# Performance work log

Hardware: AMD Instinct MI355X
Metric: run time of the kernel (lower is better)

## Reference

```python
import jax, jax.numpy as jnp
import numpy as np

B, N, F, C, K = 4, 8192, 128, 64, 16


def setup_inputs() -> dict:
    key = jax.random.key(0)
    ks = jax.random.split(key, 24)
    s = 0.05
    rn = lambda k, shape: (jax.random.normal(k, shape, jnp.float32) * s)
    return {
        "features": jax.random.normal(ks[0], (B, N, F), jnp.float32),
        "positions": jax.random.normal(ks[1], (B, N, 3), jnp.float32),
        "batch": jnp.repeat(jnp.arange(B, dtype=jnp.int32), N),
        "num_neighbors": K,
        # linear encoder (F -> C)
        "W_enc": rn(ks[2], (F, C)), "b_enc": jnp.zeros((C,), jnp.float32),
        # point-transformer q/k/v projections (C -> C)
        "Wq": rn(ks[3], (C, C)), "bq": jnp.zeros((C,), jnp.float32),
        "Wk": rn(ks[4], (C, C)), "bk": jnp.zeros((C,), jnp.float32),
        "Wv": rn(ks[5], (C, C)), "bv": jnp.zeros((C,), jnp.float32),
        # positional encoding MLP: 3 -> C -> C (ReLU)
        "Wp1": rn(ks[6], (3, C)), "bp1": jnp.zeros((C,), jnp.float32),
        "Wp2": rn(ks[7], (C, C)), "bp2": jnp.zeros((C,), jnp.float32),
        # attention MLP gamma: C -> C -> C (ReLU)
        "Wa1": rn(ks[8], (C, C)), "ba1": jnp.zeros((C,), jnp.float32),
        "Wa2": rn(ks[9], (C, C)), "ba2": jnp.zeros((C,), jnp.float32),
        # linear decoder (C -> F)
        "W_dec": rn(ks[10], (C, F)), "b_dec": jnp.zeros((F,), jnp.float32),
    }


def reference(features, positions, batch, num_neighbors,
              W_enc, b_enc, Wq, bq, Wk, bk, Wv, bv,
              Wp1, bp1, Wp2, bp2, Wa1, ba1, Wa2, ba2, W_dec, b_dec):
    # linear encode: [B,N,F] -> [B,N,C]
    x = features @ W_enc + b_enc
    q = x @ Wq + bq
    k = x @ Wk + bk
    v = x @ Wv + bv

    def per_cloud(pos, qi, ki, vi):
        # kNN via pairwise squared distances (self included, dist 0)
        sq = jnp.sum(pos * pos, axis=-1)                      # [N]
        d2 = sq[:, None] + sq[None, :] - 2.0 * (pos @ pos.T)  # [N,N]
        idx = jax.lax.top_k(-d2, num_neighbors)[1]            # [N,K]
        kj = ki[idx]                                          # [N,K,C] gather
        vj = vi[idx]                                          # [N,K,C]
        rel = pos[:, None, :] - pos[idx]                      # [N,K,3]
        # positional encoding delta = MLP(p_i - p_j)
        delta = jax.nn.relu(rel @ Wp1 + bp1) @ Wp2 + bp2      # [N,K,C]
        # vector attention: gamma(q_i - k_j + delta), softmax over K neighbors
        a = qi[:, None, :] - kj + delta
        a = jax.nn.relu(a @ Wa1 + ba1) @ Wa2 + ba2
        w = jax.nn.softmax(a, axis=1)                         # [N,K,C]
        return jnp.sum(w * (vj + delta), axis=1)              # [N,C]

    y = jax.vmap(per_cloud)(positions, q, k, v)               # [B,N,C]
    out = y @ W_dec + b_dec + features                        # decode + residual
    return (out, positions, batch)
```

## Files before the change

### kernel.cpp

```cpp
#include <hip/hip_runtime.h>
#include <hip/hip_bf16.h>

#define NPTS 32768
#define NPC  8192
#define KNN  16
#define CH   64
#define FDIM 128
#define EMPTYKEY 0x7F7FFFFFu

typedef __bf16 bf16;
typedef __bf16 bf16x2 __attribute__((ext_vector_type(2)));
typedef __bf16 bf16x8 __attribute__((ext_vector_type(8)));
typedef float  f32x4  __attribute__((ext_vector_type(4)));

__global__ __launch_bounds__(256) void k_encode(
    const float* __restrict__ feat,
    const float* __restrict__ Wenc, const float* __restrict__ benc,
    const float* __restrict__ Wq, const float* __restrict__ bq,
    const float* __restrict__ Wk, const float* __restrict__ bk,
    const float* __restrict__ Wv, const float* __restrict__ bv,
    float* __restrict__ qo, float* __restrict__ ko, float* __restrict__ vo)
{
    __shared__ float xs[4][CH];
    int t = threadIdx.x;
    int c = t & 63, pl = t >> 6;
    size_t pt = (size_t)blockIdx.x * 4 + pl;
    const float* fr = feat + pt * FDIM;
    float acc = benc[c];
#pragma unroll 8
    for (int f4 = 0; f4 < 32; ++f4) {
        float4 fv = *reinterpret_cast<const float4*>(fr + f4 * 4);
        acc += fv.x * Wenc[(f4*4+0)*CH + c];
        acc += fv.y * Wenc[(f4*4+1)*CH + c];
        acc += fv.z * Wenc[(f4*4+2)*CH + c];
        acc += fv.w * Wenc[(f4*4+3)*CH + c];
    }
    xs[pl][c] = acc;
    __syncthreads();
    float aq = bq[c], ak = bk[c], av = bv[c];
#pragma unroll 4
    for (int m = 0; m < CH; ++m) {
        float xm = xs[pl][m];
        aq += xm * Wq[m*CH + c];
        ak += xm * Wk[m*CH + c];
        av += xm * Wv[m*CH + c];
    }
    qo[pt*CH + c] = aq; ko[pt*CH + c] = ak; vo[pt*CH + c] = av;
}

__global__ __launch_bounds__(256, 4) void k_knn(
    const float* __restrict__ pos, unsigned* __restrict__ wsK)
{
    __shared__ float4 sp[1024];
    __shared__ unsigned sbuf[256 * 17];

    int t = threadIdx.x;
    int blk = blockIdx.x;
    int slice = blk & 7;
    int qg = (blk >> 3) & 31;
    int cloud = blk >> 8;
    const float* pc = pos + (size_t)cloud * NPC * 3;
    int jbase = slice << 10;

    {
        const float4* src = reinterpret_cast<const float4*>(pc + (size_t)jbase * 3);
        float4 a = src[t*3+0], b1 = src[t*3+1], c1 = src[t*3+2];
        sp[t*4+0] = make_float4(a.x,  a.y,  a.z,  0.f);
        sp[t*4+1] = make_float4(a.w,  b1.x, b1.y, 0.f);
        sp[t*4+2] = make_float4(b1.z, b1.w, c1.x, 0.f);
        sp[t*4+3] = make_float4(c1.y, c1.z, c1.w, 0.f);
    }
    __syncthreads();

    int qi = (qg << 8) + t;
    float myx = pc[qi*3+0], myy = pc[qi*3+1], myz = pc[qi*3+2];

    unsigned arr[16];
#pragma unroll
    for (int r = 0; r < 16; ++r) arr[r] = EMPTYKEY;
    float thrf = __uint_as_float(EMPTYKEY & 0xFFFFE000u);
    int cnt = 0;
    int base = t * 17;

    for (int g = 0; g < 1024; g += 4) {
        float d2v[4];
#pragma unroll
        for (int u = 0; u < 4; ++u) {
            float4 p = sp[g + u];
            float dx = myx - p.x, dy = myy - p.y, dz = myz - p.z;
            d2v[u] = dx*dx + dy*dy + dz*dz;
        }
        float m4 = fminf(fminf(d2v[0], d2v[1]), fminf(d2v[2], d2v[3]));
        if (__any(m4 <= thrf)) {
#pragma unroll
            for (int u = 0; u < 4; ++u) {
                if (d2v[u] <= thrf) {
                    sbuf[base + cnt] = (__float_as_uint(d2v[u]) & 0xFFFFE000u)
                                       | (unsigned)(jbase + g + u);
                    ++cnt;
                }
            }
            if (__any(cnt >= 13)) {
#pragma unroll
                for (int b = 0; b < 16; ++b) {
                    unsigned key = (b < cnt) ? sbuf[base + b] : EMPTYKEY;
#pragma unroll
                    for (int r = 0; r < 16; ++r) {
                        unsigned lo = min(key, arr[r]);
                        unsigned hi = max(key, arr[r]);
                        arr[r] = lo; key = hi;
                    }
                }
                cnt = 0;
                thrf = __uint_as_float(arr[15] & 0xFFFFE000u);
            }
        }
    }
#pragma unroll
    for (int b = 0; b < 16; ++b) {
        unsigned key = (b < cnt) ? sbuf[base + b] : EMPTYKEY;
#pragma unroll
        for (int r = 0; r < 16; ++r) {
            unsigned lo = min(key, arr[r]);
            unsigned hi = max(key, arr[r]);
            arr[r] = lo; key = hi;
        }
    }
    size_t gq = (size_t)cloud * NPC + qi;
#pragma unroll
    for (int r = 0; r < 16; ++r) wsK[(size_t)(slice*16 + r)*NPTS + gq] = arr[r];
}

__global__ __launch_bounds__(64) void k_merge(
    const unsigned* __restrict__ wsK, int* __restrict__ idxout,
    const float* __restrict__ Wp2, const float* __restrict__ Wa1,
    const float* __restrict__ Wa2, bf16* __restrict__ wpk)
{
    __shared__ unsigned kk[64][137];
    int t = threadIdx.x;
    size_t q = (size_t)blockIdx.x * 64 + t;
#pragma unroll
    for (int l = 0; l < 8; ++l) {
#pragma unroll
        for (int r = 0; r < 16; ++r)
            kk[t][l*17 + r] = wsK[(size_t)(l*16 + r)*NPTS + q];
        kk[t][l*17 + 16] = 0xFFFFFFFFu;
    }

    unsigned h0=0,h1=0,h2=0,h3=0,h4=0,h5=0,h6=0,h7=0;
    int* o = idxout + q * KNN;
    for (int r = 0; r < KNN; ++r) {
        unsigned best = 0xFFFFFFFFu; int bl = 0; unsigned k;
        k = kk[t][0*17 + h0]; if (k < best) { best = k; bl = 0; }
        k = kk[t][1*17 + h1]; if (k < best) { best = k; bl = 1; }
        k = kk[t][2*17 + h2]; if (k < best) { best = k; bl = 2; }
        k = kk[t][3*17 + h3]; if (k < best) { best = k; bl = 3; }
        k = kk[t][4*17 + h4]; if (k < best) { best = k; bl = 4; }
        k = kk[t][5*17 + h5]; if (k < best) { best = k; bl = 5; }
        k = kk[t][6*17 + h6]; if (k < best) { best = k; bl = 6; }
        k = kk[t][7*17 + h7]; if (k < best) { best = k; bl = 7; }
        o[r] = (int)(best & 0x1FFFu);
        h0 += (bl == 0); h1 += (bl == 1); h2 += (bl == 2); h3 += (bl == 3);
        h4 += (bl == 4); h5 += (bl == 5); h6 += (bl == 6); h7 += (bl == 7);
    }

    if (blockIdx.x == 0) {
        int lane = t;
        int mlane = lane & 15, kgrp = lane >> 4;
        const float* Ws[3] = {Wp2, Wa1, Wa2};
        bf16x8* ow = reinterpret_cast<bf16x8*>(wpk);
        for (int gmm = 0; gmm < 3; ++gmm) {
#pragma unroll
            for (int nt = 0; nt < 4; ++nt) {
#pragma unroll
                for (int kt = 0; kt < 2; ++kt) {
                    bf16x8 v;
#pragma unroll
                    for (int j = 0; j < 8; ++j)
                        v[j] = (bf16)Ws[gmm][(kt*32 + kgrp*8 + j)*CH + nt*16 + mlane];
                    ow[(gmm*8 + nt*2 + kt)*64 + lane] = v;
                }
            }
        }
    }
}

__device__ __forceinline__ void wave_gemm(
    const bf16* At, f32x4 acc[4][4], const bf16x8* __restrict__ wpk,
    int w, int lane)
{
    int kgrp = lane >> 4;
    bf16x8 wf[4][2];
#pragma unroll
    for (int nt = 0; nt < 4; ++nt)
#pragma unroll
        for (int kt = 0; kt < 2; ++kt)
            wf[nt][kt] = wpk[(nt*2 + kt)*64 + lane];
#pragma unroll
    for (int mt = 0; mt < 4; ++mt) {
        int row = w*64 + mt*16 + (lane & 15);
        const bf16* rb = At + row*CH;
        int sw = row & 7;
        bf16x8 a0 = *reinterpret_cast<const bf16x8*>(rb + ((kgrp     ^ sw) * 8));
        bf16x8 a1 = *reinterpret_cast<const bf16x8*>(rb + (((4+kgrp) ^ sw) * 8));
#pragma unroll
        for (int nt = 0; nt < 4; ++nt) {
            acc[mt][nt] = __builtin_amdgcn_mfma_f32_16x16x32_bf16(a0, wf[nt][0], acc[mt][nt], 0, 0, 0);
            acc[mt][nt] = __builtin_amdgcn_mfma_f32_16x16x32_bf16(a1, wf[nt][1], acc[mt][nt], 0, 0, 0);
        }
    }
}

__global__ __launch_bounds__(128, 3) void k_attn(
    const float* __restrict__ pos, const int* __restrict__ nidx,
    const float* __restrict__ qg, const float* __restrict__ kg, const float* __restrict__ vg,
    const float* __restrict__ Wp1, const float* __restrict__ bp1,
    const float* __restrict__ bp2, const float* __restrict__ ba1,
    const float* __restrict__ ba2, const bf16* __restrict__ wpkg,
    float* __restrict__ yout)
{
    __shared__ bf16 At[128 * CH];

    int t = threadIdx.x;
    int w = t >> 6, lane = t & 63;
    int mlane = lane & 15, kgrp = lane >> 4;
    size_t p0 = (size_t)blockIdx.x * 8;
    size_t cbase = (p0 >> 13) << 13;
    const bf16x8* wpk = reinterpret_cast<const bf16x8*>(wpkg);

    {
        int p = t >> 4, j = t & 15;
        size_t gp = p0 + p;
        int nbr = nidx[gp*KNN + j];
        size_t gn = cbase + (size_t)nbr;
        float rx = pos[gp*3+0] - pos[gn*3+0];
        float ry = pos[gp*3+1] - pos[gn*3+1];
        float rz = pos[gp*3+2] - pos[gn*3+2];
        float h[CH];
#pragma unroll
        for (int c4 = 0; c4 < 16; ++c4) {
            float4 w0 = *reinterpret_cast<const float4*>(Wp1 + 0*CH + c4*4);
            float4 w1 = *reinterpret_cast<const float4*>(Wp1 + 1*CH + c4*4);
            float4 w2 = *reinterpret_cast<const float4*>(Wp1 + 2*CH + c4*4);
            float4 bb = *reinterpret_cast<const float4*>(bp1 + c4*4);
            h[c4*4+0] = fmaxf(rx*w0.x + ry*w1.x + rz*w2.x + bb.x, 0.f);
            h[c4*4+1] = fmaxf(rx*w0.y + ry*w1.y + rz*w2.y + bb.y, 0.f);
            h[c4*4+2] = fmaxf(rx*w0.z + ry*w1.z + rz*w2.z + bb.z, 0.f);
            h[c4*4+3] = fmaxf(rx*w0.w + ry*w1.w + rz*w2.w + bb.w, 0.f);
        }
#pragma unroll
        for (int ch = 0; ch < 8; ++ch) {
            bf16x8 v;
#pragma unroll
            for (int e = 0; e < 8; ++e) v[e] = (bf16)h[ch*8 + e];
            *reinterpret_cast<bf16x8*>(&At[t*CH + (ch ^ (t & 7)) * 8]) = v;
        }
    }

    f32x4 acc[4][4];

#pragma unroll
    for (int nt = 0; nt < 4; ++nt) {
        float b = bp2[nt*16 + mlane];
#pragma unroll
        for (int mt = 0; mt < 4; ++mt) { acc[mt][nt][0]=b; acc[mt][nt][1]=b; acc[mt][nt][2]=b; acc[mt][nt][3]=b; }
    }
    wave_gemm(At, acc, wpk, w, lane);

    bf16x2 vdp[4][4][2];
#pragma unroll
    for (int mt = 0; mt < 4; ++mt) {
        size_t gp = p0 + (size_t)(w*4 + mt);
        int nb[4];
#pragma unroll
        for (int reg = 0; reg < 4; ++reg)
            nb[reg] = nidx[gp*KNN + kgrp*4 + reg];
#pragma unroll
        for (int nt = 0; nt < 4; ++nt) {
            int c = nt*16 + mlane;
            float qv = qg[gp*CH + c];
            float vdf[4];
#pragma unroll
            for (int reg = 0; reg < 4; ++reg) {
                float dlt = acc[mt][nt][reg];
                size_t gr = cbase + (size_t)nb[reg];
                float kv = kg[gr*CH + c];
                float vv = vg[gr*CH + c];
                int row = w*64 + mt*16 + kgrp*4 + reg;
                int off = row*CH + (((c >> 3) ^ (row & 7)) * 8) + (c & 7);
                At[off] = (bf16)(qv - kv + dlt);
                vdf[reg] = vv + dlt;
            }
            bf16x2 lo2; lo2[0] = (bf16)vdf[0]; lo2[1] = (bf16)vdf[1];
            bf16x2 hi2; hi2[0] = (bf16)vdf[2]; hi2[1] = (bf16)vdf[3];
            vdp[mt][nt][0] = lo2;
            vdp[mt][nt][1] = hi2;
        }
    }

#pragma unroll
    for (int nt = 0; nt < 4; ++nt) {
        float b = ba1[nt*16 + mlane];
#pragma unroll
        for (int mt = 0; mt < 4; ++mt) { acc[mt][nt][0]=b; acc[mt][nt][1]=b; acc[mt][nt][2]=b; acc[mt][nt][3]=b; }
    }
    wave_gemm(At, acc, wpk + 512, w, lane);
#pragma unroll
    for (int mt = 0; mt < 4; ++mt) {
#pragma unroll
        for (int nt = 0; nt < 4; ++nt) {
            int c = nt*16 + mlane;
#pragma unroll
            for (int reg = 0; reg < 4; ++reg) {
                int row = w*64 + mt*16 + kgrp*4 + reg;
                int off = row*CH + (((c >> 3) ^ (row & 7)) * 8) + (c & 7);
                At[off] = (bf16)fmaxf(acc[mt][nt][reg], 0.f);
            }
        }
    }

#pragma unroll
    for (int nt = 0; nt < 4; ++nt) {
        float b = ba2[nt*16 + mlane];
#pragma unroll
        for (int mt = 0; mt < 4; ++mt) { acc[mt][nt][0]=b; acc[mt][nt][1]=b; acc[mt][nt][2]=b; acc[mt][nt][3]=b; }
    }
    wave_gemm(At, acc, wpk + 1024, w, lane);

#pragma unroll
    for (int mt = 0; mt < 4; ++mt) {
        size_t gp = p0 + (size_t)(w*4 + mt);
#pragma unroll
        for (int nt = 0; nt < 4; ++nt) {
            int c = nt*16 + mlane;
            float m = fmaxf(fmaxf(acc[mt][nt][0], acc[mt][nt][1]),
                            fmaxf(acc[mt][nt][2], acc[mt][nt][3]));
            m = fmaxf(m, __shfl_xor(m, 16));
            m = fmaxf(m, __shfl_xor(m, 32));
            float e[4], s = 0.f;
#pragma unroll
            for (int reg = 0; reg < 4; ++reg) { e[reg] = __expf(acc[mt][nt][reg] - m); s += e[reg]; }
            s += __shfl_xor(s, 16);
            s += __shfl_xor(s, 32);
            float num = 0.f;
            num += e[0] * (float)vdp[mt][nt][0][0];
            num += e[1] * (float)vdp[mt][nt][0][1];
            num += e[2] * (float)vdp[mt][nt][1][0];
            num += e[3] * (float)vdp[mt][nt][1][1];
            num += __shfl_xor(num, 16);
            num += __shfl_xor(num, 32);
            if (kgrp == 0) yout[gp*CH + c] = num / s;
        }
    }
}

__global__ __launch_bounds__(256) void k_decode(
    const float* __restrict__ y, const float* __restrict__ Wd, const float* __restrict__ bd,
    const float* __restrict__ feat, const float* __restrict__ pos,
    const int* __restrict__ batch, float* __restrict__ out)
{
    int t = threadIdx.x;
    int f = t & 127, pl = t >> 7;
    size_t pt = (size_t)blockIdx.x * 2 + pl;
    const float* yr = y + pt*CH;
    float acc = bd[f] + feat[pt*FDIM + f];
#pragma unroll
    for (int c4 = 0; c4 < 16; ++c4) {
        float4 yv = *reinterpret_cast<const float4*>(yr + c4*4);
        acc += yv.x * Wd[(c4*4+0)*FDIM + f];
        acc += yv.y * Wd[(c4*4+1)*FDIM + f];
        acc += yv.z * Wd[(c4*4+2)*FDIM + f];
        acc += yv.w * Wd[(c4*4+3)*FDIM + f];
    }
    out[pt*FDIM + f] = acc;

    int i = blockIdx.x * 256 + t;
    if (i < NPTS*3) out[(size_t)NPTS*FDIM + i] = pos[i];
    if (i < NPTS)   out[(size_t)NPTS*FDIM + NPTS*3 + i] = (float)batch[i];
}

extern "C" void kernel_launch(void* const* d_in, const int* in_sizes, int n_in,
                              void* d_out, int out_size, void* d_ws, size_t ws_size,
                              hipStream_t stream)
{
    const float* feat  = (const float*)d_in[0];
    const float* pos   = (const float*)d_in[1];
    const int*   batch = (const int*)d_in[2];
    const float* Wenc  = (const float*)d_in[4];
    const float* benc  = (const float*)d_in[5];
    const float* Wq = (const float*)d_in[6];   const float* bq = (const float*)d_in[7];
    const float* Wk = (const float*)d_in[8];   const float* bk = (const float*)d_in[9];
    const float* Wv = (const float*)d_in[10];  const float* bv = (const float*)d_in[11];
    const float* Wp1= (const float*)d_in[12];  const float* bp1= (const float*)d_in[13];
    const float* Wp2= (const float*)d_in[14];  const float* bp2= (const float*)d_in[15];
    const float* Wa1= (const float*)d_in[16];  const float* ba1= (const float*)d_in[17];
    const float* Wa2= (const float*)d_in[18];  const float* ba2= (const float*)d_in[19];
    const float* Wd = (const float*)d_in[20];  const float* bd = (const float*)d_in[21];
    float* out = (float*)d_out;

    int*      idx = (int*)d_ws;
    unsigned* wsK = (unsigned*)((char*)d_ws + (size_t)NPTS*KNN*sizeof(int));
    float* qb = (float*)wsK;
    float* kb = qb + (size_t)NPTS*CH;
    float* vb = kb + (size_t)NPTS*CH;
    float* yb = vb + (size_t)NPTS*CH;
    bf16*  wpk = (bf16*)(yb + (size_t)NPTS*CH);

    k_knn<<<1024, 256, 0, stream>>>(pos, wsK);
    k_merge<<<NPTS/64, 64, 0, stream>>>(wsK, idx, Wp2, Wa1, Wa2, wpk);

    k_encode<<<NPTS/4, 256, 0, stream>>>(feat, Wenc, benc, Wq, bq, Wk, bk, Wv, bv, qb, kb, vb);

    k_attn<<<NPTS/8, 128, 0, stream>>>(pos, idx, qb, kb, vb,
                                       Wp1, bp1, bp2, ba1, ba2, wpk, yb);

    k_decode<<<NPTS/2, 256, 0, stream>>>(yb, Wd, bd, feat, pos, batch, out);
}
```

Before: 468.0 us.

## Store q/k/v in bf16 with interleaved k/v, skip useless kNN inserts, remap attn blocks

The encoder now writes q as bf16 and k/v as interleaved bf16 pairs, so the attention gather fetches k and v in one 4-byte load and moves half the bytes. The kNN insertion network is skipped when a candidate key is not smaller than the current 16th-best entry. The attention grid is remapped so that blocks landing on the same XCD work on the same cloud, which should improve L2 locality for the neighbour gathers. Rounding q/k/v to bf16 lowers accuracy, and the early-exit branch can diverge within a wave.

```diff
diff --git a/kernel.cpp b/kernel.cpp
--- a/kernel.cpp
+++ b/kernel.cpp
@@ -19,7 +19,7 @@
     const float* __restrict__ Wq, const float* __restrict__ bq,
     const float* __restrict__ Wk, const float* __restrict__ bk,
     const float* __restrict__ Wv, const float* __restrict__ bv,
-    float* __restrict__ qo, float* __restrict__ ko, float* __restrict__ vo)
+    bf16* __restrict__ qo, bf16* __restrict__ kvo)
 {
     __shared__ float xs[4][CH];
     int t = threadIdx.x;
@@ -45,7 +45,9 @@
         ak += xm * Wk[m*CH + c];
         av += xm * Wv[m*CH + c];
     }
-    qo[pt*CH + c] = aq; ko[pt*CH + c] = ak; vo[pt*CH + c] = av;
+    qo[pt*CH + c] = (bf16)aq;
+    bf16x2 kv2; kv2[0] = (bf16)ak; kv2[1] = (bf16)av;
+    *reinterpret_cast<bf16x2*>(&kvo[pt*2*CH + 2*c]) = kv2;
 }
 
 __global__ __launch_bounds__(256, 4) void k_knn(
@@ -104,11 +106,13 @@
 #pragma unroll
                 for (int b = 0; b < 16; ++b) {
                     unsigned key = (b < cnt) ? sbuf[base + b] : EMPTYKEY;
-#pragma unroll
-                    for (int r = 0; r < 16; ++r) {
-                        unsigned lo = min(key, arr[r]);
-                        unsigned hi = max(key, arr[r]);
-                        arr[r] = lo; key = hi;
+                    if (key < arr[15]) {
+#pragma unroll
+                        for (int r = 0; r < 16; ++r) {
+                            unsigned lo = min(key, arr[r]);
+                            unsigned hi = max(key, arr[r]);
+                            arr[r] = lo; key = hi;
+                        }
                     }
                 }
                 cnt = 0;
@@ -119,11 +123,13 @@
 #pragma unroll
     for (int b = 0; b < 16; ++b) {
         unsigned key = (b < cnt) ? sbuf[base + b] : EMPTYKEY;
-#pragma unroll
-        for (int r = 0; r < 16; ++r) {
-            unsigned lo = min(key, arr[r]);
-            unsigned hi = max(key, arr[r]);
-            arr[r] = lo; key = hi;
+        if (key < arr[15]) {
+#pragma unroll
+            for (int r = 0; r < 16; ++r) {
+                unsigned lo = min(key, arr[r]);
+                unsigned hi = max(key, arr[r]);
+                arr[r] = lo; key = hi;
+            }
         }
     }
     size_t gq = (size_t)cloud * NPC + qi;
@@ -213,7 +219,7 @@
 
 __global__ __launch_bounds__(128, 3) void k_attn(
     const float* __restrict__ pos, const int* __restrict__ nidx,
-    const float* __restrict__ qg, const float* __restrict__ kg, const float* __restrict__ vg,
+    const bf16* __restrict__ qg, const bf16* __restrict__ kvg,
     const float* __restrict__ Wp1, const float* __restrict__ bp1,
     const float* __restrict__ bp2, const float* __restrict__ ba1,
     const float* __restrict__ ba2, const bf16* __restrict__ wpkg,
@@ -224,8 +230,13 @@
     int t = threadIdx.x;
     int w = t >> 6, lane = t & 63;
     int mlane = lane & 15, kgrp = lane >> 4;
-    size_t p0 = (size_t)blockIdx.x * 8;
-    size_t cbase = (p0 >> 13) << 13;
+    int blk = blockIdx.x;
+    int xcd = blk & 7;
+    int cloud = xcd >> 1;
+    int sub = ((blk >> 3) << 1) | (xcd & 1);
+    size_t cbase = (size_t)cloud * NPC;
+    size_t p0 = cbase + (size_t)sub * 8;
+    const bf16x2* kv2 = reinterpret_cast<const bf16x2*>(kvg);
     const bf16x8* wpk = reinterpret_cast<const bf16x8*>(wpkg);
 
     {
@@ -278,17 +289,18 @@
 #pragma unroll
         for (int nt = 0; nt < 4; ++nt) {
             int c = nt*16 + mlane;
-            float qv = qg[gp*CH + c];
+            float qv = (float)qg[gp*CH + c];
             float vdf[4];
 #pragma unroll
             for (int reg = 0; reg < 4; ++reg) {
                 float dlt = acc[mt][nt][reg];
                 size_t gr = cbase + (size_t)nb[reg];
-                float kv = kg[gr*CH + c];
-                float vv = vg[gr*CH + c];
+                bf16x2 kvp = kv2[gr*CH + c];
+                float kvf = (float)kvp[0];
+                float vv  = (float)kvp[1];
                 int row = w*64 + mt*16 + kgrp*4 + reg;
                 int off = row*CH + (((c >> 3) ^ (row & 7)) * 8) + (c & 7);
-                At[off] = (bf16)(qv - kv + dlt);
+                At[off] = (bf16)(qv - kvf + dlt);
                 vdf[reg] = vv + dlt;
             }
             bf16x2 lo2; lo2[0] = (bf16)vdf[0]; lo2[1] = (bf16)vdf[1];
@@ -400,18 +412,17 @@
 
     int*      idx = (int*)d_ws;
     unsigned* wsK = (unsigned*)((char*)d_ws + (size_t)NPTS*KNN*sizeof(int));
-    float* qb = (float*)wsK;
-    float* kb = qb + (size_t)NPTS*CH;
-    float* vb = kb + (size_t)NPTS*CH;
-    float* yb = vb + (size_t)NPTS*CH;
+    bf16* qb  = (bf16*)wsK;
+    bf16* kvb = qb + (size_t)NPTS*CH;
+    float* yb = (float*)((char*)wsK + (size_t)NPTS*KNN*8*sizeof(unsigned));
     bf16*  wpk = (bf16*)(yb + (size_t)NPTS*CH);
 
     k_knn<<<1024, 256, 0, stream>>>(pos, wsK);
     k_merge<<<NPTS/64, 64, 0, stream>>>(wsK, idx, Wp2, Wa1, Wa2, wpk);
 
-    k_encode<<<NPTS/4, 256, 0, stream>>>(feat, Wenc, benc, Wq, bq, Wk, bk, Wv, bv, qb, kb, vb);
-
-    k_attn<<<NPTS/8, 128, 0, stream>>>(pos, idx, qb, kb, vb,
+    k_encode<<<NPTS/4, 256, 0, stream>>>(feat, Wenc, benc, Wq, bq, Wk, bk, Wv, bv, qb, kvb);
+
+    k_attn<<<NPTS/8, 128, 0, stream>>>(pos, idx, qb, kvb,
                                        Wp1, bp1, bp2, ba1, ba2, wpk, yb);
 
     k_decode<<<NPTS/2, 256, 0, stream>>>(yb, Wd, bd, feat, pos, batch, out);
```

Result: no change. 465.3 us (-0.6%).
